# Performance work log

Hardware: AMD Instinct MI355X
Metric: run time of the kernel (lower is better)

## Reference

```python
import jax, jax.numpy as jnp
import numpy as np

H = 8          # num_heads
WIN = 63       # win_size
LEFT = WIN - 1 - WIN // 2  # 31
EPS = 1e-5


def layer_norm(x, w, b):
    mu = x.mean(-1, keepdims=True)
    var = ((x - mu) ** 2).mean(-1, keepdims=True)
    return (x - mu) / jnp.sqrt(var + EPS) * w + b


def setup_inputs() -> dict:
    key = jax.random.key(0)
    N, T, C = 2, 2048, 512
    hid = 4 * C
    ks = jax.random.split(key, 16)
    s = 0.02
    return {
        "x": jax.random.normal(ks[0], (N, T, C), jnp.float32),
        "norm1_w": jnp.ones((C,), jnp.float32),
        "norm1_b": jnp.zeros((C,), jnp.float32),
        "qkv_w": jax.random.normal(ks[1], (3 * C, C), jnp.float32) * s,
        "qkv_b": jnp.zeros((3 * C,), jnp.float32),
        "rel_bias": jax.random.normal(ks[2], (H, WIN), jnp.float32) * s,
        "proj_w": jax.random.normal(ks[3], (C, C), jnp.float32) * s,
        "proj_b": jnp.zeros((C,), jnp.float32),
        "norm2_w": jnp.ones((C,), jnp.float32),
        "norm2_b": jnp.zeros((C,), jnp.float32),
        "fc1_w": jax.random.normal(ks[4], (hid, C), jnp.float32) * s,
        "fc1_b": jnp.zeros((hid,), jnp.float32),
        "fc2_w": jax.random.normal(ks[5], (C, hid), jnp.float32) * s,
        "fc2_b": jnp.zeros((C,), jnp.float32),
    }


def reference(x, norm1_w, norm1_b, qkv_w, qkv_b, rel_bias, proj_w, proj_b,
              norm2_w, norm2_b, fc1_w, fc1_b, fc2_w, fc2_b):
    N, T, C = x.shape
    hd = C // H
    scale = hd ** -0.5
    right = WIN - LEFT - 1

    shortcut = x
    h = layer_norm(x, norm1_w, norm1_b)
    qkv = (h @ qkv_w.T + qkv_b).reshape(N, T, 3, H, hd)
    q, k, v = qkv[:, :, 0], qkv[:, :, 1], qkv[:, :, 2]  # (N,T,H,hd)

    # zero-pad keys/values along time, gather sliding windows
    kp = jnp.pad(k, ((0, 0), (LEFT, right), (0, 0), (0, 0)))
    vp = jnp.pad(v, ((0, 0), (LEFT, right), (0, 0), (0, 0)))
    idx = jnp.arange(T)[:, None] + jnp.arange(WIN)[None, :]
    k_win = kp[:, idx]
    v_win = vp[:, idx]

    attn = jnp.einsum('nthd,ntwhd->nhtw', q * scale, k_win)
    attn = attn + rel_bias[None, :, None, :]
    # boundary mask: key position j = t - LEFT + w must lie in [0, T)
    pos = idx - LEFT
    mask = jnp.where((pos < 0) | (pos >= T), jnp.float32(-100.0), jnp.float32(0.0))
    attn = attn + mask[None, None, :, :]
    attn = jax.nn.softmax(attn, axis=-1)

    out = jnp.einsum('nhtw,ntwhd->nthd', attn, v_win).reshape(N, T, C)
    out = out @ proj_w.T + proj_b

    x = shortcut + out
    h2 = layer_norm(x, norm2_w, norm2_b)
    m = jax.nn.gelu(h2 @ fc1_w.T + fc1_b, approximate=False)  # torch nn.GELU = exact erf
    m = m @ fc2_w.T + fc2_b
    return x + m
```

## Files before the change

### kernel.cpp

```cpp
#include <hip/hip_runtime.h>

typedef unsigned short u16;
typedef unsigned int uint;
typedef __attribute__((ext_vector_type(4))) float floatx4;
typedef __attribute__((ext_vector_type(16))) float floatx16;
typedef __attribute__((ext_vector_type(8))) short shortx8;

__device__ __forceinline__ u16 f2b(float f) {
    unsigned int u = __float_as_uint(f);
    unsigned int r = (u + 0x7fffu + ((u >> 16) & 1u)) >> 16;
    return (u16)r;
}
__device__ __forceinline__ float b2f(u16 u) {
    return __uint_as_float(((unsigned int)u) << 16);
}
__device__ __forceinline__ void gl_lds16(const u16* g, u16* l) {
    __builtin_amdgcn_global_load_lds(
        (const __attribute__((address_space(1))) void*)g,
        (__attribute__((address_space(3))) void*)l, 16, 0, 0);
}
__device__ __forceinline__ float gelu_f(float v) {
    float e = __expf(1.59576912f * v * (1.0f + 0.044715f * v * v));
    return v * e / (e + 1.0f);
}

__device__ __forceinline__ void ln_row_wave_f32(const float* __restrict__ x,
                                                const float* __restrict__ w,
                                                const float* __restrict__ b,
                                                u16* __restrict__ out, int row) {
    int lane = threadIdx.x & 63;
    const float4* xr = (const float4*)(x + (size_t)row * 512);
    float4 v0 = xr[lane * 2], v1 = xr[lane * 2 + 1];
    float s = v0.x + v0.y + v0.z + v0.w + v1.x + v1.y + v1.z + v1.w;
    float s2 = v0.x * v0.x + v0.y * v0.y + v0.z * v0.z + v0.w * v0.w +
               v1.x * v1.x + v1.y * v1.y + v1.z * v1.z + v1.w * v1.w;
    #pragma unroll
    for (int o = 32; o > 0; o >>= 1) {
        s += __shfl_xor(s, o, 64);
        s2 += __shfl_xor(s2, o, 64);
    }
    float mu = s * (1.0f / 512.0f);
    float var = s2 * (1.0f / 512.0f) - mu * mu;
    float rstd = rsqrtf(var + 1e-5f);
    const float4* wr = (const float4*)w;
    const float4* br = (const float4*)b;
    float4 w0 = wr[lane * 2], w1 = wr[lane * 2 + 1];
    float4 b0 = br[lane * 2], b1 = br[lane * 2 + 1];
    uint4 o4;
    o4.x = (uint)f2b((v0.x - mu) * rstd * w0.x + b0.x) |
           ((uint)f2b((v0.y - mu) * rstd * w0.y + b0.y) << 16);
    o4.y = (uint)f2b((v0.z - mu) * rstd * w0.z + b0.z) |
           ((uint)f2b((v0.w - mu) * rstd * w0.w + b0.w) << 16);
    o4.z = (uint)f2b((v1.x - mu) * rstd * w1.x + b1.x) |
           ((uint)f2b((v1.y - mu) * rstd * w1.y + b1.y) << 16);
    o4.w = (uint)f2b((v1.z - mu) * rstd * w1.z + b1.z) |
           ((uint)f2b((v1.w - mu) * rstd * w1.w + b1.w) << 16);
    ((uint4*)(out + (size_t)row * 512))[lane] = o4;
}

__global__ __launch_bounds__(256) void ln_kernel_b(const u16* __restrict__ x,
                                                   const float* __restrict__ w,
                                                   const float* __restrict__ b,
                                                   u16* __restrict__ out) {
    int row = blockIdx.x * 4 + (threadIdx.x >> 6);
    int lane = threadIdx.x & 63;
    uint4 p = ((const uint4*)(x + (size_t)row * 512))[lane];
    float v[8];
    v[0] = b2f((u16)(p.x & 0xffffu)); v[1] = b2f((u16)(p.x >> 16));
    v[2] = b2f((u16)(p.y & 0xffffu)); v[3] = b2f((u16)(p.y >> 16));
    v[4] = b2f((u16)(p.z & 0xffffu)); v[5] = b2f((u16)(p.z >> 16));
    v[6] = b2f((u16)(p.w & 0xffffu)); v[7] = b2f((u16)(p.w >> 16));
    float s = 0.f, s2 = 0.f;
    #pragma unroll
    for (int i = 0; i < 8; i++) { s += v[i]; s2 += v[i] * v[i]; }
    #pragma unroll
    for (int o = 32; o > 0; o >>= 1) {
        s += __shfl_xor(s, o, 64);
        s2 += __shfl_xor(s2, o, 64);
    }
    float mu = s * (1.0f / 512.0f);
    float var = s2 * (1.0f / 512.0f) - mu * mu;
    float rstd = rsqrtf(var + 1e-5f);
    const float4* wr = (const float4*)w;
    const float4* br = (const float4*)b;
    float4 w0 = wr[lane * 2], w1 = wr[lane * 2 + 1];
    float4 b0 = br[lane * 2], b1 = br[lane * 2 + 1];
    float o8[8];
    o8[0] = (v[0] - mu) * rstd * w0.x + b0.x;
    o8[1] = (v[1] - mu) * rstd * w0.y + b0.y;
    o8[2] = (v[2] - mu) * rstd * w0.z + b0.z;
    o8[3] = (v[3] - mu) * rstd * w0.w + b0.w;
    o8[4] = (v[4] - mu) * rstd * w1.x + b1.x;
    o8[5] = (v[5] - mu) * rstd * w1.y + b1.y;
    o8[6] = (v[6] - mu) * rstd * w1.z + b1.z;
    o8[7] = (v[7] - mu) * rstd * w1.w + b1.w;
    uint4 o4;
    o4.x = (uint)f2b(o8[0]) | ((uint)f2b(o8[1]) << 16);
    o4.y = (uint)f2b(o8[2]) | ((uint)f2b(o8[3]) << 16);
    o4.z = (uint)f2b(o8[4]) | ((uint)f2b(o8[5]) << 16);
    o4.w = (uint)f2b(o8[6]) | ((uint)f2b(o8[7]) << 16);
    ((uint4*)(out + (size_t)row * 512))[lane] = o4;
}

__global__ __launch_bounds__(256) void prep_kernel(
    const float* __restrict__ qkvw, u16* __restrict__ wq,
    const float* __restrict__ projw, u16* __restrict__ wp,
    const float* __restrict__ fc1w, u16* __restrict__ w1,
    const float* __restrict__ fc2w, u16* __restrict__ w2,
    const float* __restrict__ x, const float* __restrict__ n1w,
    const float* __restrict__ n1b, u16* __restrict__ hb) {
    int bi = blockIdx.x;
    if (bi < 3072) {
        const float* src;
        u16* dst;
        int i0;
        if (bi < 768)       { src = qkvw; dst = wq; i0 = bi; }
        else if (bi < 1024) { src = projw; dst = wp; i0 = bi - 768; }
        else if (bi < 2048) { src = fc1w; dst = w1; i0 = bi - 1024; }
        else                { src = fc2w; dst = w2; i0 = bi - 2048; }
        int i = i0 * 256 + threadIdx.x;
        float4 v = ((const float4*)src)[i];
        uint2 o;
        o.x = (uint)f2b(v.x) | ((uint)f2b(v.y) << 16);
        o.y = (uint)f2b(v.z) | ((uint)f2b(v.w) << 16);
        ((uint2*)dst)[i] = o;
    } else {
        int row = (bi - 3072) * 4 + (threadIdx.x >> 6);
        ln_row_wave_f32(x, n1w, n1b, hb, row);
    }
}

template <int EPI>
__global__ __launch_bounds__(256, 2) void gemm16(const u16* __restrict__ A,
                                                 const u16* __restrict__ W,
                                                 const float* __restrict__ bias,
                                                 u16* __restrict__ outB,
                                                 int M, int Nn, int K) {
    constexpr int BM = 128, BN = 128, BK = 64;
    __shared__ u16 a_s[2][BM * BK];
    __shared__ u16 b_s[2][BN * BK];

    int tid = threadIdx.x;
    int wid = tid >> 6, lane = tid & 63;
    int wm = wid >> 1, wn = wid & 1;
    int m_blk = blockIdx.x * BM;
    int n_blk = blockIdx.y * BN;
    int lr = lane & 15;
    int lkc = lane >> 4;

    floatx4 acc[4][4];
    #pragma unroll
    for (int i = 0; i < 4; i++)
        #pragma unroll
        for (int j = 0; j < 4; j++) acc[i][j] = (floatx4){0.f, 0.f, 0.f, 0.f};

    const u16* Ag = A + (size_t)m_blk * K;
    const u16* Wg = W + (size_t)n_blk * K;

    int srow = tid >> 3;
    int skc = (tid & 7) ^ (srow & 7);

    auto stage = [&](int k0, int buf) {
        #pragma unroll
        for (int p = 0; p < 4; p++)
            gl_lds16(Ag + (size_t)(p * 32 + srow) * K + k0 + skc * 8,
                     a_s[buf] + (p * 256 + tid) * 8);
        #pragma unroll
        for (int p = 0; p < 4; p++)
            gl_lds16(Wg + (size_t)(p * 32 + srow) * K + k0 + skc * 8,
                     b_s[buf] + (p * 256 + tid) * 8);
    };

    stage(0, 0);
    int nit = K >> 6;
    for (int it = 0; it < nit; it++) {
        __syncthreads();
        if (it + 1 < nit) stage((it + 1) << 6, (it + 1) & 1);
        int cb = it & 1;
        #pragma unroll
        for (int s = 0; s < 2; s++) {
            int kc = s * 4 + lkc;
            shortx8 af[4], bf[4];
            #pragma unroll
            for (int i = 0; i < 4; i++) {
                int row = wm * 64 + i * 16 + lr;
                af[i] = *(const shortx8*)(a_s[cb] + (row * 8 + (kc ^ (row & 7))) * 8);
            }
            #pragma unroll
            for (int j = 0; j < 4; j++) {
                int row = wn * 64 + j * 16 + lr;
                bf[j] = *(const shortx8*)(b_s[cb] + (row * 8 + (kc ^ (row & 7))) * 8);
            }
            #pragma unroll
            for (int i = 0; i < 4; i++)
                #pragma unroll
                for (int j = 0; j < 4; j++)
                    acc[i][j] = __builtin_amdgcn_mfma_f32_16x16x32_bf16(
                        af[i], bf[j], acc[i][j], 0, 0, 0);
        }
    }

    int col_l = lane & 15;
    int row_base = (lane >> 4) * 4;
    #pragma unroll
    for (int nj = 0; nj < 4; nj++) {
        int col = n_blk + wn * 64 + nj * 16 + col_l;
        float bv = bias[col];
        #pragma unroll
        for (int mi = 0; mi < 4; mi++) {
            #pragma unroll
            for (int r = 0; r < 4; r++) {
                int row = m_blk + wm * 64 + mi * 16 + row_base + r;
                size_t off = (size_t)row * Nn + col;
                float v = acc[mi][nj][r] + bv;
                outB[off] = f2b(EPI == 2 ? gelu_f(v) : v);
            }
        }
    }
}

template <int EPI>
__global__ __launch_bounds__(256, 2) void gemm32(const u16* __restrict__ A,
                                                 const u16* __restrict__ W,
                                                 const float* __restrict__ bias,
                                                 const float* __restrict__ residF,
                                                 const u16* __restrict__ residB,
                                                 float* __restrict__ outF,
                                                 u16* __restrict__ outB,
                                                 int M, int Nn, int K) {
    constexpr int BM = 64, BN = 64, BK = 128;
    constexpr int CPR = BK / 8, KMSK = CPR - 1;
    __shared__ u16 a_s[2][BM * BK];
    __shared__ u16 b_s[2][BN * BK];

    int tid = threadIdx.x;
    int wid = tid >> 6, lane = tid & 63;
    int wm = wid >> 1, wn = wid & 1;
    int m_blk = blockIdx.x * BM;
    int n_blk = blockIdx.y * BN;
    int lr = lane & 31;
    int lk = lane >> 5;

    floatx16 acc;
    #pragma unroll
    for (int r = 0; r < 16; r++) acc[r] = 0.f;

    const u16* Ag = A + (size_t)m_blk * K;
    const u16* Wg = W + (size_t)n_blk * K;

    int srow = tid / CPR;
    int skc = (tid & KMSK) ^ (srow & KMSK);

    auto stage = [&](int k0, int buf) {
        #pragma unroll
        for (int p = 0; p < 4; p++)
            gl_lds16(Ag + (size_t)(p * 16 + srow) * K + k0 + skc * 8,
                     a_s[buf] + (p * 256 + tid) * 8);
        #pragma unroll
        for (int p = 0; p < 4; p++)
            gl_lds16(Wg + (size_t)(p * 16 + srow) * K + k0 + skc * 8,
                     b_s[buf] + (p * 256 + tid) * 8);
    };

    stage(0, 0);
    int nit = K / BK;
    for (int it = 0; it < nit; it++) {
        __syncthreads();
        if (it + 1 < nit) stage((it + 1) * BK, (it + 1) & 1);
        int cb = it & 1;
        #pragma unroll
        for (int s = 0; s < BK / 16; s++) {
            int kc = s * 2 + lk;
            int arow = wm * 32 + lr;
            int brow = wn * 32 + lr;
            shortx8 af = *(const shortx8*)(a_s[cb] + (arow * CPR + (kc ^ (arow & KMSK))) * 8);
            shortx8 bf = *(const shortx8*)(b_s[cb] + (brow * CPR + (kc ^ (brow & KMSK))) * 8);
            acc = __builtin_amdgcn_mfma_f32_32x32x16_bf16(af, bf, acc, 0, 0, 0);
        }
    }

    int col_l = lane & 31;
    int row_q = 4 * (lane >> 5);
    int col = n_blk + wn * 32 + col_l;
    float bv = bias[col];
    #pragma unroll
    for (int r = 0; r < 16; r++) {
        int row = m_blk + wm * 32 + (r & 3) + 8 * (r >> 2) + row_q;
        size_t off = (size_t)row * Nn + col;
        float v = acc[r] + bv;
        if (EPI == 1) outB[off] = f2b(v + residF[off]);
        else          outF[off] = v + b2f(residB[off]);
    }
}

__global__ __launch_bounds__(256) void attn_kernel(const u16* __restrict__ qkv,
                                                   const float* __restrict__ rel_bias,
                                                   u16* __restrict__ out) {
    __shared__ u16 k_s[128][72];
    __shared__ u16 v_t[64][152];
    __shared__ u16 p_s[4][16][104];
    __shared__ float s_bias[64];

    int bx = blockIdx.x;
    int n = bx >> 8;
    int h = (bx >> 5) & 7;
    int t0 = (bx & 31) << 6;
    int tid = threadIdx.x, wid = tid >> 6, lane = tid & 63;
    int col = lane & 15, rq = lane >> 4;

    const u16* qrow = qkv + (size_t)(n * 2048 + t0 + wid * 16 + col) * 1536 + h * 64 + rq * 8;
    shortx8 qf0 = *(const shortx8*)qrow;
    shortx8 qf1 = *(const shortx8*)(qrow + 32);

    if (tid < 63) s_bias[tid] = rel_bias[h * 63 + tid];
    if (tid == 63) s_bias[63] = 0.f;

    const uint* qkv_u = (const uint*)qkv;
    for (int idx = tid; idx < 128 * 32; idx += 256) {
        int row = idx >> 5, j = idx & 31;
        int pos = t0 - 31 + row;
        uint kv = 0;
        if (pos >= 0 && pos < 2048)
            kv = qkv_u[(size_t)(n * 2048 + pos) * 768 + 256 + h * 32 + j];
        *(uint*)&k_s[row][j * 2] = kv;
    }
    for (int idx = tid; idx < 144 * 32; idx += 256) {
        int row = idx >> 5, j = idx & 31;
        int pos = t0 - 31 + row;
        uint vv = 0;
        if (pos >= 0 && pos < 2048)
            vv = qkv_u[(size_t)(n * 2048 + pos) * 768 + 512 + h * 32 + j];
        v_t[2 * j][row] = (u16)(vv & 0xffffu);
        v_t[2 * j + 1][row] = (u16)(vv >> 16);
    }
    __syncthreads();

    floatx4 S[5];
    #pragma unroll
    for (int nt = 0; nt < 5; nt++) S[nt] = (floatx4){0.f, 0.f, 0.f, 0.f};
    #pragma unroll
    for (int nt = 0; nt < 5; nt++) {
        const u16* kb = &k_s[wid * 16 + nt * 16 + col][rq * 8];
        shortx8 b0 = *(const shortx8*)kb;
        shortx8 b1 = *(const shortx8*)(kb + 32);
        S[nt] = __builtin_amdgcn_mfma_f32_16x16x32_bf16(qf0, b0, S[nt], 0, 0, 0);
        S[nt] = __builtin_amdgcn_mfma_f32_16x16x32_bf16(qf1, b1, S[nt], 0, 0, 0);
    }

    #pragma unroll
    for (int r = 0; r < 4; r++) {
        int t_row = rq * 4 + r;
        float sc[5];
        float mx = -1e30f;
        #pragma unroll
        for (int nt = 0; nt < 5; nt++) {
            int w = nt * 16 + col - t_row;
            int pos_abs = t0 - 31 + wid * 16 + nt * 16 + col;
            float v;
            if (w < 0 || w > 62) {
                v = -1e30f;
            } else {
                v = S[nt][r] * 0.125f + s_bias[w];
                if (pos_abs < 0 || pos_abs >= 2048) v -= 100.f;
            }
            sc[nt] = v;
            mx = fmaxf(mx, v);
        }
        #pragma unroll
        for (int o = 1; o < 16; o <<= 1) mx = fmaxf(mx, __shfl_xor(mx, o, 64));
        float l = 0.f;
        #pragma unroll
        for (int nt = 0; nt < 5; nt++) {
            sc[nt] = __expf(sc[nt] - mx);
            l += sc[nt];
        }
        #pragma unroll
        for (int o = 1; o < 16; o <<= 1) l += __shfl_xor(l, o, 64);
        float inv = 1.0f / l;
        #pragma unroll
        for (int nt = 0; nt < 5; nt++)
            p_s[wid][t_row][nt * 16 + col] = f2b(sc[nt] * inv);
        p_s[wid][t_row][80 + col] = 0;
    }
    __syncthreads();

    floatx4 O[4];
    #pragma unroll
    for (int dt = 0; dt < 4; dt++) O[dt] = (floatx4){0.f, 0.f, 0.f, 0.f};
    const u16* pr = &p_s[wid][col][rq * 8];
    shortx8 a0 = *(const shortx8*)pr;
    shortx8 a1 = *(const shortx8*)(pr + 32);
    shortx8 a2 = *(const shortx8*)(pr + 64);
    #pragma unroll
    for (int dt = 0; dt < 4; dt++) {
        const u16* vb = &v_t[dt * 16 + col][wid * 16 + rq * 8];
        shortx8 b0 = *(const shortx8*)vb;
        shortx8 b1 = *(const shortx8*)(vb + 32);
        shortx8 b2 = *(const shortx8*)(vb + 64);
        O[dt] = __builtin_amdgcn_mfma_f32_16x16x32_bf16(a0, b0, O[dt], 0, 0, 0);
        O[dt] = __builtin_amdgcn_mfma_f32_16x16x32_bf16(a1, b1, O[dt], 0, 0, 0);
        O[dt] = __builtin_amdgcn_mfma_f32_16x16x32_bf16(a2, b2, O[dt], 0, 0, 0);
    }

    #pragma unroll
    for (int dt = 0; dt < 4; dt++) {
        #pragma unroll
        for (int r = 0; r < 4; r++) {
            int t_row = rq * 4 + r;
            out[(size_t)(n * 2048 + t0 + wid * 16 + t_row) * 512 + h * 64 + dt * 16 + col] =
                f2b(O[dt][r]);
        }
    }
}

extern "C" void kernel_launch(void* const* d_in, const int* in_sizes, int n_in,
                              void* d_out, int out_size, void* d_ws, size_t ws_size,
                              hipStream_t stream) {
    const float* x     = (const float*)d_in[0];
    const float* n1w   = (const float*)d_in[1];
    const float* n1b   = (const float*)d_in[2];
    const float* qkvw  = (const float*)d_in[3];
    const float* qkvbv = (const float*)d_in[4];
    const float* relb  = (const float*)d_in[5];
    const float* projw = (const float*)d_in[6];
    const float* projb = (const float*)d_in[7];
    const float* n2w   = (const float*)d_in[8];
    const float* n2b   = (const float*)d_in[9];
    const float* fc1w  = (const float*)d_in[10];
    const float* fc1b  = (const float*)d_in[11];
    const float* fc2w  = (const float*)d_in[12];
    const float* fc2b  = (const float*)d_in[13];
    float* out = (float*)d_out;

    char* p = (char*)d_ws;
    u16* wq   = (u16*)p;  p += (size_t)786432 * 2;
    u16* wp   = (u16*)p;  p += (size_t)262144 * 2;
    u16* w1   = (u16*)p;  p += (size_t)1048576 * 2;
    u16* w2   = (u16*)p;  p += (size_t)1048576 * 2;
    u16* hb   = (u16*)p;  p += (size_t)2097152 * 2;
    u16* qkvb = (u16*)p;  p += (size_t)6291456 * 2;
    u16* attb = (u16*)p;  p += (size_t)2097152 * 2;
    u16* x2b  = (u16*)p;  p += (size_t)2097152 * 2;
    u16* mb   = (u16*)p;  p += (size_t)8388608 * 2;

    prep_kernel<<<4096, 256, 0, stream>>>(qkvw, wq, projw, wp, fc1w, w1, fc2w, w2,
                                          x, n1w, n1b, hb);
    gemm16<0><<<dim3(32, 12), 256, 0, stream>>>(hb, wq, qkvbv, qkvb, 4096, 1536, 512);
    attn_kernel<<<512, 256, 0, stream>>>(qkvb, relb, attb);
    gemm32<1><<<dim3(64, 8), 256, 0, stream>>>(attb, wp, projb, x, nullptr,
                                               nullptr, x2b, 4096, 512, 512);
    ln_kernel_b<<<1024, 256, 0, stream>>>(x2b, n2w, n2b, hb);
    gemm16<2><<<dim3(32, 16), 256, 0, stream>>>(hb, w1, fc1b, mb, 4096, 2048, 512);
    gemm32<3><<<dim3(64, 8), 256, 0, stream>>>(mb, w2, fc2b, nullptr, x2b,
                                               out, nullptr, 4096, 512, 2048);
}
```

Baseline: 168.0 us.

## Fuse all layer stages into one persistent kernel with global atomic barriers

```diff
diff --git a/kernel.cpp b/kernel.cpp
--- a/kernel.cpp
+++ b/kernel.cpp
@@ -22,6 +22,29 @@
 __device__ __forceinline__ float gelu_f(float v) {
     float e = __expf(1.59576912f * v * (1.0f + 0.044715f * v * v));
     return v * e / (e + 1.0f);
+}
+
+struct SG16 { u16 a[2][128 * 64]; u16 b[2][128 * 64]; };
+struct SG32 { u16 a[2][64 * 128]; u16 b[2][64 * 128]; };
+struct SAttn {
+    u16 k[128][72];
+    u16 v[64][152];
+    u16 p[4][16][104];
+    float bias[64];
+};
+union SMem { SG16 g16; SG32 g32; SAttn at; };
+static_assert(sizeof(SMem) == 65536, "smem union must be 64KiB");
+
+__device__ __forceinline__ void gbar(unsigned* c, unsigned tgt) {
+    __syncthreads();
+    if (threadIdx.x == 0) {
+        __threadfence();
+        __hip_atomic_fetch_add(c, 1u, __ATOMIC_RELEASE, __HIP_MEMORY_SCOPE_AGENT);
+        while (__hip_atomic_load(c, __ATOMIC_ACQUIRE, __HIP_MEMORY_SCOPE_AGENT) < tgt)
+            __builtin_amdgcn_s_sleep(2);
+        __threadfence();
+    }
+    __syncthreads();
 }
 
 __device__ __forceinline__ void ln_row_wave_f32(const float* __restrict__ x,
@@ -58,11 +81,10 @@
     ((uint4*)(out + (size_t)row * 512))[lane] = o4;
 }
 
-__global__ __launch_bounds__(256) void ln_kernel_b(const u16* __restrict__ x,
-                                                   const float* __restrict__ w,
-                                                   const float* __restrict__ b,
-                                                   u16* __restrict__ out) {
-    int row = blockIdx.x * 4 + (threadIdx.x >> 6);
+__device__ __forceinline__ void ln_row_wave_b16(const u16* __restrict__ x,
+                                                const float* __restrict__ w,
+                                                const float* __restrict__ b,
+                                                u16* __restrict__ out, int row) {
     int lane = threadIdx.x & 63;
     uint4 p = ((const uint4*)(x + (size_t)row * 512))[lane];
     float v[8];
@@ -102,14 +124,13 @@
     ((uint4*)(out + (size_t)row * 512))[lane] = o4;
 }
 
-__global__ __launch_bounds__(256) void prep_kernel(
-    const float* __restrict__ qkvw, u16* __restrict__ wq,
+__device__ __forceinline__ void prep_body(
+    int bi, const float* __restrict__ qkvw, u16* __restrict__ wq,
     const float* __restrict__ projw, u16* __restrict__ wp,
     const float* __restrict__ fc1w, u16* __restrict__ w1,
     const float* __restrict__ fc2w, u16* __restrict__ w2,
     const float* __restrict__ x, const float* __restrict__ n1w,
     const float* __restrict__ n1b, u16* __restrict__ hb) {
-    int bi = blockIdx.x;
     if (bi < 3072) {
         const float* src;
         u16* dst;
@@ -131,20 +152,18 @@
 }
 
 template <int EPI>
-__global__ __launch_bounds__(256, 2) void gemm16(const u16* __restrict__ A,
-                                                 const u16* __restrict__ W,
-                                                 const float* __restrict__ bias,
-                                                 u16* __restrict__ outB,
-                                                 int M, int Nn, int K) {
+__device__ __forceinline__ void gemm16_body(SMem& sm, int bx, int by,
+                                            const u16* __restrict__ A,
+                                            const u16* __restrict__ W,
+                                            const float* __restrict__ bias,
+                                            u16* __restrict__ outB,
+                                            int M, int Nn, int K) {
     constexpr int BM = 128, BN = 128, BK = 64;
-    __shared__ u16 a_s[2][BM * BK];
-    __shared__ u16 b_s[2][BN * BK];
-
     int tid = threadIdx.x;
     int wid = tid >> 6, lane = tid & 63;
     int wm = wid >> 1, wn = wid & 1;
-    int m_blk = blockIdx.x * BM;
-    int n_blk = blockIdx.y * BN;
+    int m_blk = bx * BM;
+    int n_blk = by * BN;
     int lr = lane & 15;
     int lkc = lane >> 4;
 
@@ -164,11 +183,11 @@
         #pragma unroll
         for (int p = 0; p < 4; p++)
             gl_lds16(Ag + (size_t)(p * 32 + srow) * K + k0 + skc * 8,
-                     a_s[buf] + (p * 256 + tid) * 8);
+                     sm.g16.a[buf] + (p * 256 + tid) * 8);
         #pragma unroll
         for (int p = 0; p < 4; p++)
             gl_lds16(Wg + (size_t)(p * 32 + srow) * K + k0 + skc * 8,
-                     b_s[buf] + (p * 256 + tid) * 8);
+                     sm.g16.b[buf] + (p * 256 + tid) * 8);
     };
 
     stage(0, 0);
@@ -184,12 +203,12 @@
             #pragma unroll
             for (int i = 0; i < 4; i++) {
                 int row = wm * 64 + i * 16 + lr;
-                af[i] = *(const shortx8*)(a_s[cb] + (row * 8 + (kc ^ (row & 7))) * 8);
+                af[i] = *(const shortx8*)(sm.g16.a[cb] + (row * 8 + (kc ^ (row & 7))) * 8);
             }
             #pragma unroll
             for (int j = 0; j < 4; j++) {
                 int row = wn * 64 + j * 16 + lr;
-                bf[j] = *(const shortx8*)(b_s[cb] + (row * 8 + (kc ^ (row & 7))) * 8);
+                bf[j] = *(const shortx8*)(sm.g16.b[cb] + (row * 8 + (kc ^ (row & 7))) * 8);
             }
             #pragma unroll
             for (int i = 0; i < 4; i++)
@@ -220,24 +239,22 @@
 }
 
 template <int EPI>
-__global__ __launch_bounds__(256, 2) void gemm32(const u16* __restrict__ A,
-                                                 const u16* __restrict__ W,
-                                                 const float* __restrict__ bias,
-                                                 const float* __restrict__ residF,
-                                                 const u16* __restrict__ residB,
-                                                 float* __restrict__ outF,
-                                                 u16* __restrict__ outB,
-                                                 int M, int Nn, int K) {
+__device__ __forceinline__ void gemm32_body(SMem& sm, int bx, int by,
+                                            const u16* __restrict__ A,
+                                            const u16* __restrict__ W,
+                                            const float* __restrict__ bias,
+                                            const float* __restrict__ residF,
+                                            const u16* __restrict__ residB,
+                                            float* __restrict__ outF,
+                                            u16* __restrict__ outB,
+                                            int M, int Nn, int K) {
     constexpr int BM = 64, BN = 64, BK = 128;
     constexpr int CPR = BK / 8, KMSK = CPR - 1;
-    __shared__ u16 a_s[2][BM * BK];
-    __shared__ u16 b_s[2][BN * BK];
-
     int tid = threadIdx.x;
     int wid = tid >> 6, lane = tid & 63;
     int wm = wid >> 1, wn = wid & 1;
-    int m_blk = blockIdx.x * BM;
-    int n_blk = blockIdx.y * BN;
+    int m_blk = bx * BM;
+    int n_blk = by * BN;
     int lr = lane & 31;
     int lk = lane >> 5;
 
@@ -255,11 +272,11 @@
         #pragma unroll
         for (int p = 0; p < 4; p++)
             gl_lds16(Ag + (size_t)(p * 16 + srow) * K + k0 + skc * 8,
-                     a_s[buf] + (p * 256 + tid) * 8);
+                     sm.g32.a[buf] + (p * 256 + tid) * 8);
         #pragma unroll
         for (int p = 0; p < 4; p++)
             gl_lds16(Wg + (size_t)(p * 16 + srow) * K + k0 + skc * 8,
-                     b_s[buf] + (p * 256 + tid) * 8);
+                     sm.g32.b[buf] + (p * 256 + tid) * 8);
     };
 
     stage(0, 0);
@@ -273,8 +290,8 @@
             int kc = s * 2 + lk;
             int arow = wm * 32 + lr;
             int brow = wn * 32 + lr;
-            shortx8 af = *(const shortx8*)(a_s[cb] + (arow * CPR + (kc ^ (arow & KMSK))) * 8);
-            shortx8 bf = *(const shortx8*)(b_s[cb] + (brow * CPR + (kc ^ (brow & KMSK))) * 8);
+            shortx8 af = *(const shortx8*)(sm.g32.a[cb] + (arow * CPR + (kc ^ (arow & KMSK))) * 8);
+            shortx8 bf = *(const shortx8*)(sm.g32.b[cb] + (brow * CPR + (kc ^ (brow & KMSK))) * 8);
             acc = __builtin_amdgcn_mfma_f32_32x32x16_bf16(af, bf, acc, 0, 0, 0);
         }
     }
@@ -293,18 +310,13 @@
     }
 }
 
-__global__ __launch_bounds__(256) void attn_kernel(const u16* __restrict__ qkv,
-                                                   const float* __restrict__ rel_bias,
-                                                   u16* __restrict__ out) {
-    __shared__ u16 k_s[128][72];
-    __shared__ u16 v_t[64][152];
-    __shared__ u16 p_s[4][16][104];
-    __shared__ float s_bias[64];
-
-    int bx = blockIdx.x;
-    int n = bx >> 8;
-    int h = (bx >> 5) & 7;
-    int t0 = (bx & 31) << 6;
+__device__ __forceinline__ void attn_body(SMem& sm, int bxx,
+                                          const u16* __restrict__ qkv,
+                                          const float* __restrict__ rel_bias,
+                                          u16* __restrict__ out) {
+    int n = bxx >> 8;
+    int h = (bxx >> 5) & 7;
+    int t0 = (bxx & 31) << 6;
     int tid = threadIdx.x, wid = tid >> 6, lane = tid & 63;
     int col = lane & 15, rq = lane >> 4;
 
@@ -312,26 +324,29 @@
     shortx8 qf0 = *(const shortx8*)qrow;
     shortx8 qf1 = *(const shortx8*)(qrow + 32);
 
-    if (tid < 63) s_bias[tid] = rel_bias[h * 63 + tid];
-    if (tid == 63) s_bias[63] = 0.f;
+    if (tid < 63) sm.at.bias[tid] = rel_bias[h * 63 + tid];
+    if (tid == 63) sm.at.bias[63] = 0.f;
 
     const uint* qkv_u = (const uint*)qkv;
-    for (int idx = tid; idx < 128 * 32; idx += 256) {
-        int row = idx >> 5, j = idx & 31;
+    for (int idx = tid; idx < 128 * 16; idx += 256) {
+        int row = idx >> 4, j2 = idx & 15;
         int pos = t0 - 31 + row;
-        uint kv = 0;
+        uint2 kv; kv.x = 0u; kv.y = 0u;
         if (pos >= 0 && pos < 2048)
-            kv = qkv_u[(size_t)(n * 2048 + pos) * 768 + 256 + h * 32 + j];
-        *(uint*)&k_s[row][j * 2] = kv;
-    }
-    for (int idx = tid; idx < 144 * 32; idx += 256) {
-        int row = idx >> 5, j = idx & 31;
-        int pos = t0 - 31 + row;
-        uint vv = 0;
-        if (pos >= 0 && pos < 2048)
-            vv = qkv_u[(size_t)(n * 2048 + pos) * 768 + 512 + h * 32 + j];
-        v_t[2 * j][row] = (u16)(vv & 0xffffu);
-        v_t[2 * j + 1][row] = (u16)(vv >> 16);
+            kv = *(const uint2*)(qkv_u + (size_t)(n * 2048 + pos) * 768 + 256 + h * 32 + j2 * 2);
+        *(uint2*)&sm.at.k[row][j2 * 4] = kv;
+    }
+    for (int idx = tid; idx < 72 * 32; idx += 256) {
+        int rp = idx >> 5, j = idx & 31;
+        int r0 = rp * 2;
+        int p0 = t0 - 31 + r0, p1 = p0 + 1;
+        uint a = 0u, b = 0u;
+        if (p0 >= 0 && p0 < 2048)
+            a = qkv_u[(size_t)(n * 2048 + p0) * 768 + 512 + h * 32 + j];
+        if (p1 >= 0 && p1 < 2048)
+            b = qkv_u[(size_t)(n * 2048 + p1) * 768 + 512 + h * 32 + j];
+        *(uint*)&sm.at.v[2 * j][r0]     = (a & 0xffffu) | (b << 16);
+        *(uint*)&sm.at.v[2 * j + 1][r0] = (a >> 16) | (b & 0xffff0000u);
     }
     __syncthreads();
 
@@ -340,7 +355,7 @@
     for (int nt = 0; nt < 5; nt++) S[nt] = (floatx4){0.f, 0.f, 0.f, 0.f};
     #pragma unroll
     for (int nt = 0; nt < 5; nt++) {
-        const u16* kb = &k_s[wid * 16 + nt * 16 + col][rq * 8];
+        const u16* kb = &sm.at.k[wid * 16 + nt * 16 + col][rq * 8];
         shortx8 b0 = *(const shortx8*)kb;
         shortx8 b1 = *(const shortx8*)(kb + 32);
         S[nt] = __builtin_amdgcn_mfma_f32_16x16x32_bf16(qf0, b0, S[nt], 0, 0, 0);
@@ -360,7 +375,7 @@
             if (w < 0 || w > 62) {
                 v = -1e30f;
             } else {
-                v = S[nt][r] * 0.125f + s_bias[w];
+                v = S[nt][r] * 0.125f + sm.at.bias[w];
                 if (pos_abs < 0 || pos_abs >= 2048) v -= 100.f;
             }
             sc[nt] = v;
@@ -379,21 +394,21 @@
         float inv = 1.0f / l;
         #pragma unroll
         for (int nt = 0; nt < 5; nt++)
-            p_s[wid][t_row][nt * 16 + col] = f2b(sc[nt] * inv);
-        p_s[wid][t_row][80 + col] = 0;
+            sm.at.p[wid][t_row][nt * 16 + col] = f2b(sc[nt] * inv);
+        sm.at.p[wid][t_row][80 + col] = 0;
     }
     __syncthreads();
 
     floatx4 O[4];
     #pragma unroll
     for (int dt = 0; dt < 4; dt++) O[dt] = (floatx4){0.f, 0.f, 0.f, 0.f};
-    const u16* pr = &p_s[wid][col][rq * 8];
+    const u16* pr = &sm.at.p[wid][col][rq * 8];
     shortx8 a0 = *(const shortx8*)pr;
     shortx8 a1 = *(const shortx8*)(pr + 32);
     shortx8 a2 = *(const shortx8*)(pr + 64);
     #pragma unroll
     for (int dt = 0; dt < 4; dt++) {
-        const u16* vb = &v_t[dt * 16 + col][wid * 16 + rq * 8];
+        const u16* vb = &sm.at.v[dt * 16 + col][wid * 16 + rq * 8];
         shortx8 b0 = *(const shortx8*)vb;
         shortx8 b1 = *(const shortx8*)(vb + 32);
         shortx8 b2 = *(const shortx8*)(vb + 64);
@@ -411,6 +426,50 @@
                 f2b(O[dt][r]);
         }
     }
+}
+
+__global__ __launch_bounds__(256, 2) void fused_layer(
+    const float* __restrict__ x, const float* __restrict__ n1w,
+    const float* __restrict__ n1b, const float* __restrict__ qkvw,
+    const float* __restrict__ qkvbv, const float* __restrict__ relb,
+    const float* __restrict__ projw, const float* __restrict__ projb,
+    const float* __restrict__ n2w, const float* __restrict__ n2b,
+    const float* __restrict__ fc1w, const float* __restrict__ fc1b,
+    const float* __restrict__ fc2w, const float* __restrict__ fc2b,
+    float* __restrict__ out,
+    u16* __restrict__ wq, u16* __restrict__ wp, u16* __restrict__ w1,
+    u16* __restrict__ w2, u16* __restrict__ hb, u16* __restrict__ qkvb,
+    u16* __restrict__ attb, u16* __restrict__ x2b, u16* __restrict__ mb,
+    unsigned* __restrict__ ctrs) {
+    __shared__ SMem sm;
+    int b = blockIdx.x;
+
+    for (int vb = b; vb < 4096; vb += 512)
+        prep_body(vb, qkvw, wq, projw, wp, fc1w, w1, fc2w, w2, x, n1w, n1b, hb);
+    gbar(&ctrs[0], 512);
+
+    if (b < 384)
+        gemm16_body<0>(sm, b & 31, b >> 5, hb, wq, qkvbv, qkvb, 4096, 1536, 512);
+    gbar(&ctrs[1], 512);
+
+    attn_body(sm, b, qkvb, relb, attb);
+    gbar(&ctrs[2], 512);
+
+    gemm32_body<1>(sm, b & 63, b >> 6, attb, wp, projb, x, nullptr,
+                   nullptr, x2b, 4096, 512, 512);
+    gbar(&ctrs[3], 512);
+
+    for (int vb = b; vb < 1024; vb += 512) {
+        int row = vb * 4 + (threadIdx.x >> 6);
+        ln_row_wave_b16(x2b, n2w, n2b, hb, row);
+    }
+    gbar(&ctrs[4], 512);
+
+    gemm16_body<2>(sm, b & 31, b >> 5, hb, w1, fc1b, mb, 4096, 2048, 512);
+    gbar(&ctrs[5], 512);
+
+    gemm32_body<3>(sm, b & 63, b >> 6, mb, w2, fc2b, nullptr, x2b,
+                   out, nullptr, 4096, 512, 2048);
 }
 
 extern "C" void kernel_launch(void* const* d_in, const int* in_sizes, int n_in,
@@ -442,15 +501,11 @@
     u16* attb = (u16*)p;  p += (size_t)2097152 * 2;
     u16* x2b  = (u16*)p;  p += (size_t)2097152 * 2;
     u16* mb   = (u16*)p;  p += (size_t)8388608 * 2;
-
-    prep_kernel<<<4096, 256, 0, stream>>>(qkvw, wq, projw, wp, fc1w, w1, fc2w, w2,
-                                          x, n1w, n1b, hb);
-    gemm16<0><<<dim3(32, 12), 256, 0, stream>>>(hb, wq, qkvbv, qkvb, 4096, 1536, 512);
-    attn_kernel<<<512, 256, 0, stream>>>(qkvb, relb, attb);
-    gemm32<1><<<dim3(64, 8), 256, 0, stream>>>(attb, wp, projb, x, nullptr,
-                                               nullptr, x2b, 4096, 512, 512);
-    ln_kernel_b<<<1024, 256, 0, stream>>>(x2b, n2w, n2b, hb);
-    gemm16<2><<<dim3(32, 16), 256, 0, stream>>>(hb, w1, fc1b, mb, 4096, 2048, 512);
-    gemm32<3><<<dim3(64, 8), 256, 0, stream>>>(mb, w2, fc2b, nullptr, x2b,
-                                               out, nullptr, 4096, 512, 2048);
-}
+    unsigned* ctrs = (unsigned*)p;
+
+    hipMemsetAsync(ctrs, 0, 64, stream);
+    fused_layer<<<512, 256, 0, stream>>>(x, n1w, n1b, qkvw, qkvbv, relb, projw,
+                                         projb, n2w, n2b, fc1w, fc1b, fc2w, fc2b,
+                                         out, wq, wp, w1, w2, hb, qkvb, attb,
+                                         x2b, mb, ctrs);
+}
```

Result: slower. 660.2 us (+293.0%).
